# Optimization experiments

Hardware: AMD Instinct MI355X
Metric: run time of the kernel (lower is better)

Reference implementation:

```python
import jax, jax.numpy as jnp
import numpy as np

B, P, E, D, A, M, V, T = 64, 196, 2048, 512, 512, 512, 10000, 31


def setup_inputs() -> dict:
    key = jax.random.key(0)
    ks = jax.random.split(key, 20)
    s = 0.02
    inp = {
        "encoder_out": jax.random.normal(ks[0], (B, P, E), jnp.float32),
        "captions": jax.random.randint(ks[1], (B, T), 0, V),
        "caption_lengths": jax.random.randint(ks[2], (B,), 2, T + 1).at[0].set(T),
        # parameters
        "W_emb": jax.random.normal(ks[3], (V, M), jnp.float32) * s,
        "We": jax.random.normal(ks[4], (A, E), jnp.float32) * s,
        "be": jnp.zeros((A,), jnp.float32),
        "Wd": jax.random.normal(ks[5], (A, D), jnp.float32) * s,
        "bd": jnp.zeros((A,), jnp.float32),
        "wf": jax.random.normal(ks[6], (1, A), jnp.float32) * s,
        "bf": jnp.zeros((1,), jnp.float32),
        "Wih": jax.random.normal(ks[7], (4 * D, M + E), jnp.float32) * s,
        "bih": jnp.zeros((4 * D,), jnp.float32),
        "Whh": jax.random.normal(ks[8], (4 * D, D), jnp.float32) * s,
        "bhh": jnp.zeros((4 * D,), jnp.float32),
        "Wfc": jax.random.normal(ks[9], (V, D), jnp.float32) * s,
        "bfc": jnp.zeros((V,), jnp.float32),
        "Wh0": jax.random.normal(ks[10], (D, E), jnp.float32) * s,
        "bh0": jnp.zeros((D,), jnp.float32),
        "Wc0": jax.random.normal(ks[11], (D, E), jnp.float32) * s,
        "bc0": jnp.zeros((D,), jnp.float32),
    }
    return inp


def _decode(encoder_out, W_emb, We, be, Wd, bd, wf, bf, Wih, bih, Whh, bhh,
            Wfc, bfc, Wh0, bh0, Wc0, bc0, captions, caption_lengths):
    # sort by length descending (matches torch .sort(descending=True))
    idx = jnp.argsort(-caption_lengths)
    lens = caption_lengths[idx]
    enc = encoder_out[idx]              # [B,P,E]
    caps = captions[idx]                # [B,T]
    emb = W_emb[caps]                   # [B,T,M]
    mean_enc = enc.mean(axis=1)         # [B,E]
    h0 = mean_enc @ Wh0.T + bh0         # [B,D]
    c0 = mean_enc @ Wc0.T + bc0
    dec_len = lens - 1                  # [B]
    att1 = enc @ We.T + be              # [B,P,A] precomputed encoder projection
    Tmax = caps.shape[1] - 1

    def step(carry, xs):
        h, c = carry
        e_t, t = xs                     # e_t: [B,M]
        active = (t < dec_len)          # [B]
        att2 = h @ Wd.T + bd            # [B,A]
        scores = jnp.tanh(att1 + att2[:, None, :]) @ wf[0] + bf[0]  # [B,P]
        alpha = jax.nn.softmax(scores, axis=-1)                      # [B,P]
        ctx = jnp.einsum('bp,bpe->be', alpha, enc)                   # [B,E]
        x = jnp.concatenate([e_t, ctx], axis=-1)                     # [B,M+E]
        gates = x @ Wih.T + bih + h @ Whh.T + bhh                    # [B,4D]
        i_g, f_g, g_g, o_g = jnp.split(gates, 4, axis=-1)
        c_t = jax.nn.sigmoid(f_g) * c + jax.nn.sigmoid(i_g) * jnp.tanh(g_g)
        h_t = jax.nn.sigmoid(o_g) * jnp.tanh(c_t)
        pred = h_t @ Wfc.T + bfc        # dropout in eval mode = identity
        m = active[:, None]
        h_new = jnp.where(m, h_t, h)
        c_new = jnp.where(m, c_t, c)
        pred = jnp.where(m, pred, 0.0)
        alpha = jnp.where(m, alpha, 0.0)
        return (h_new, c_new), (pred, alpha)

    emb_ts = jnp.swapaxes(emb[:, :Tmax, :], 0, 1)  # [Tmax,B,M]
    ts = jnp.arange(Tmax)
    _, (preds, alphas) = jax.lax.scan(step, (h0, c0), (emb_ts, ts))
    predictions = jnp.swapaxes(preds, 0, 1)   # [B,Tmax,V]
    alphas = jnp.swapaxes(alphas, 0, 1)       # [B,Tmax,P]
    return predictions, alphas


def reference(encoder_out, captions, caption_lengths, W_emb, We, be, Wd, bd,
              wf, bf, Wih, bih, Whh, bhh, Wfc, bfc, Wh0, bh0, Wc0, bc0):
    return _decode(encoder_out, W_emb, We, be, Wd, bd, wf, bf, Wih, bih,
                   Whh, bhh, Wfc, bfc, Wh0, bh0, Wc0, bc0,
                   captions, caption_lengths)
```

## Files before the change

kernel.cpp:

```cpp
#include <hip/hip_runtime.h>
#include <cstdint>
#include <cstddef>

typedef __attribute__((ext_vector_type(8))) short short8;
typedef __attribute__((ext_vector_type(4))) float f32x4;

#define DEV static __device__ __forceinline__

#define PRED_ELEMS 19200000ULL

#define OFF_ENC   0ULL
#define OFF_ATT1  51380224ULL
#define OFF_B1    64225280ULL
#define OFF_WFC   69468160ULL
#define OFF_WEB   79724544ULL
#define OFF_B0    81821696ULL
#define OFF_HH    81821696ULL
#define OFF_B2    86016000ULL
#define OFF_HX    94404608ULL
#define OFF_C     94535680ULL
#define OFF_ATT2  94666752ULL
#define OFF_GEH   94797824ULL
#define OFF_SC    95322112ULL
#define OFF_CTX   95372288ULL
#define OFF_META  95634432ULL

DEV float b2f(unsigned short u){ unsigned v = ((unsigned)u) << 16; float f; __builtin_memcpy(&f, &v, 4); return f; }
DEV unsigned short f2b(float x){ unsigned v; __builtin_memcpy(&v, &x, 4); unsigned r = v + 0x7fffu + ((v >> 16) & 1u); return (unsigned short)(r >> 16); }
DEV float sigm(float x){ return 1.0f / (1.0f + __expf(-x)); }
DEV float tanhf_fast(float x){ float e = __expf(2.0f * x); return 1.0f - 2.0f / (e + 1.0f); }

DEV void gload16(const void* g, void* l){
  __builtin_amdgcn_global_load_lds((const __attribute__((address_space(1))) unsigned int*)g,
                                   (__attribute__((address_space(3))) unsigned int*)l, 16, 0, 0);
}

DEV void mm_core(const unsigned short* A, int ldA, int m0,
                 const unsigned short* Bm, int ldB, int n0,
                 int kIters, unsigned short* As, unsigned short* Bs, f32x4 acc[4])
{
  const int tid = threadIdx.x;
  const int lane = tid & 63, w = tid >> 6;
  const unsigned short* ga = A + (size_t)(m0 + lane) * ldA + w * 8;
  const unsigned short* gb = Bm + (size_t)(n0 + lane) * ldB + w * 8;
  unsigned short* la = As + w * 512;
  unsigned short* lb = Bs + w * 512;
  const int kb = lane >> 4, rr = lane & 15;
  for (int kk = 0; kk < kIters; ++kk) {
    gload16(ga, la); gload16(gb, lb);
    ga += 32; gb += 32;
    asm volatile("s_waitcnt vmcnt(0)" ::: "memory");
    __syncthreads();
    short8 bfr = *(const short8*)(Bs + (size_t)(kb * 64 + w * 16 + rr) * 8);
#pragma unroll
    for (int f = 0; f < 4; ++f) {
      short8 afr = *(const short8*)(As + (size_t)(kb * 64 + f * 16 + rr) * 8);
      acc[f] = __builtin_amdgcn_mfma_f32_16x16x32_bf16(afr, bfr, acc[f], 0, 0, 0);
    }
    __syncthreads();
  }
}

__global__ void k_meta(const int* __restrict__ caps, const int* __restrict__ lens, int* __restrict__ meta){
  int j = threadIdx.x;
  int lj = lens[j];
  int rank = 0;
  for (int k = 0; k < 64; ++k) { int lk = lens[k]; rank += (lk > lj) || (lk == lj && k < j); }
  meta[rank] = j; meta[64 + rank] = lj - 1;
  for (int t = 0; t < 31; ++t) meta[160 + rank * 31 + t] = caps[j * 31 + t];
  __syncthreads();
  if (j < 30) { int c = 0; for (int b = 0; b < 64; ++b) c += (meta[64 + b] > j); meta[128 + j] = c; }
}

__global__ __launch_bounds__(256) void k_encg(const float* __restrict__ enc, const int* __restrict__ meta, unsigned short* __restrict__ encb){
  int row = blockIdx.x; int b = row / 196, p = row % 196;
  const float* src = enc + ((size_t)meta[b] * 196 + p) * 2048;
  unsigned short* dst = encb + (size_t)row * 2048;
  int e0 = threadIdx.x * 8;
  short8 o;
#pragma unroll
  for (int j = 0; j < 8; ++j) o[j] = (short)f2b(src[e0 + j]);
  *(short8*)(dst + e0) = o;
}

__global__ __launch_bounds__(256) void k_wconv(const float* We, const float* Wh0, const float* Wc0,
                        const float* Wd, const float* Whh, const float* Wih, const float* Wfc,
                        unsigned short* Web, unsigned short* B0, unsigned short* B1,
                        unsigned short* Wfcb, unsigned short* B2){
  int bid = blockIdx.x, tid = threadIdx.x;
  if (bid < 512) {
    const float* s = We + (size_t)bid * 2048; unsigned short* d = Web + (size_t)bid * 2048;
    int e0 = tid * 8; short8 o;
#pragma unroll
    for (int j = 0; j < 8; ++j) o[j] = (short)f2b(s[e0 + j]);
    *(short8*)(d + e0) = o;
  } else if (bid < 1536) {
    int r = bid - 512;
    const float* s = (r < 512) ? (Wh0 + (size_t)r * 2048) : (Wc0 + (size_t)(r - 512) * 2048);
    unsigned short* d = B0 + (size_t)r * 2048;
    int e0 = tid * 8; short8 o;
#pragma unroll
    for (int j = 0; j < 8; ++j) o[j] = (short)f2b(s[e0 + j]);
    *(short8*)(d + e0) = o;
  } else if (bid < 3584) {
    int jr = bid - 1536; int g = (jr & 3) * 512 + (jr >> 2);
    const float* s = Wih + (size_t)g * 2560 + 512;
    unsigned short* d = B2 + (size_t)jr * 2048;
    int e0 = tid * 8; short8 o;
#pragma unroll
    for (int j = 0; j < 8; ++j) o[j] = (short)f2b(s[e0 + j]);
    *(short8*)(d + e0) = o;
  } else if (bid < 6144) {
    int n = bid - 3584; unsigned short* d = B1 + (size_t)n * 1024;
    int k0 = tid * 4;
    if (n < 512) {
#pragma unroll
      for (int j = 0; j < 4; ++j) { int k = k0 + j; d[k] = (k < 512) ? f2b(Wd[(size_t)n * 512 + k]) : (unsigned short)0; }
    } else {
      int j2 = n - 512; int g = (j2 & 3) * 512 + (j2 >> 2);
#pragma unroll
      for (int j = 0; j < 4; ++j) { int k = k0 + j;
        d[k] = (k < 512) ? f2b(Whh[(size_t)g * 512 + k]) : f2b(Wih[(size_t)g * 2560 + (k - 512)]); }
    }
  } else {
    int v = bid - 6144; unsigned short* d = Wfcb + (size_t)v * 512;
    int k0 = tid * 2;
#pragma unroll
    for (int j = 0; j < 2; ++j) d[k0 + j] = (v < 10000) ? f2b(Wfc[(size_t)v * 512 + k0 + j]) : (unsigned short)0;
  }
}

__global__ __launch_bounds__(256) void k_mean(const unsigned short* __restrict__ encb, unsigned short* __restrict__ meanb){
  int b = blockIdx.y, ch = blockIdx.x;
  int e = ch * 512 + threadIdx.x * 2;
  const unsigned short* ep = encb + (size_t)b * 196 * 2048 + e;
  float s0 = 0.f, s1 = 0.f;
  for (int p = 0; p < 196; ++p) {
    unsigned u = *(const unsigned*)(ep + (size_t)p * 2048);
    s0 += b2f((unsigned short)(u & 0xffff));
    s1 += b2f((unsigned short)(u >> 16));
  }
  const float inv = 1.0f / 196.0f;
  unsigned o = ((unsigned)f2b(s1 * inv) << 16) | f2b(s0 * inv);
  *(unsigned*)(meanb + (size_t)b * 2048 + e) = o;
}

__global__ __launch_bounds__(256) void k_h0c0(const unsigned short* meanb, const unsigned short* B0,
                      const float* bh0, const float* bc0, unsigned short* hx, float* cbuf){
  __shared__ __align__(16) unsigned short As[2048], Bs[2048];
  f32x4 acc[4];
#pragma unroll
  for (int f = 0; f < 4; ++f) acc[f] = (f32x4){0.f,0.f,0.f,0.f};
  int nt = blockIdx.x;
  mm_core(meanb, 2048, 0, B0, 2048, nt * 64, 64, As, Bs, acc);
  int lane = threadIdx.x & 63, w = threadIdx.x >> 6;
  int col = lane & 15, rhi = lane >> 4;
  int n = nt * 64 + w * 16 + col;
#pragma unroll
  for (int f = 0; f < 4; ++f)
#pragma unroll
    for (int r = 0; r < 4; ++r) {
      int b = f * 16 + rhi * 4 + r; float v = acc[f][r];
      if (n < 512) hx[(size_t)b * 1024 + n] = f2b(v + bh0[n]);
      else cbuf[(size_t)b * 512 + (n - 512)] = v + bc0[n - 512];
    }
}

__global__ void k_emb0(const float* __restrict__ Wemb, const int* __restrict__ meta, unsigned short* __restrict__ hx){
  int b = blockIdx.x;
  int cap = meta[160 + b * 31];
  for (int j = threadIdx.x; j < 512; j += 256)
    hx[(size_t)b * 1024 + 512 + j] = f2b(Wemb[(size_t)cap * 512 + j]);
}

__global__ __launch_bounds__(256) void k_att1(const unsigned short* __restrict__ encb,
                      const unsigned short* __restrict__ Web,
                      const float* __restrict__ be, unsigned short* __restrict__ att1b){
  __shared__ __align__(16) unsigned short As[2][4096], Bs[2][4096];
  int tid = threadIdx.x, lane = tid & 63, w = tid >> 6;
  int bid = blockIdx.x, mt, nt;
  if (bid < 384) { mt = (bid >> 5) * 8 + (bid & 7); nt = (bid >> 3) & 3; }
  else           { mt = 96 + ((bid - 384) >> 2);    nt = (bid - 384) & 3; }
  int wr = (w >> 1) * 64, wc = (w & 1) * 64;
  int rr = lane & 15, kb = lane >> 4;
  f32x4 acc[4][4];
#pragma unroll
  for (int f = 0; f < 4; ++f)
#pragma unroll
    for (int q = 0; q < 4; ++q) acc[f][q] = (f32x4){0.f,0.f,0.f,0.f};

  const unsigned short* gA = encb + (size_t)mt * 128 * 2048;
  const unsigned short* gB = Web + (size_t)nt * 128 * 2048;
  int L0 = tid, L1 = tid + 256;
  size_t s0 = (size_t)(L0 & 127) * 2048 + ((L0 >> 7) << 3);
  size_t s1 = (size_t)(L1 & 127) * 2048 + ((L1 >> 7) << 3);
  int d0 = (w * 64) * 8, d1 = (w * 64 + 256) * 8;

#define STAGE_A1(kk, bf) do { \
    gload16(gA + s0 + (size_t)(kk) * 32, &As[bf][d0]); \
    gload16(gB + s0 + (size_t)(kk) * 32, &Bs[bf][d0]); \
    gload16(gA + s1 + (size_t)(kk) * 32, &As[bf][d1]); \
    gload16(gB + s1 + (size_t)(kk) * 32, &Bs[bf][d1]); \
  } while (0)

  STAGE_A1(0, 0);
  __syncthreads();
  for (int kk = 0; kk < 64; ++kk) {
    int cur = kk & 1;
    if (kk < 63) STAGE_A1(kk + 1, cur ^ 1);
    short8 af[4], bq[4];
#pragma unroll
    for (int f = 0; f < 4; ++f)
      af[f] = *(const short8*)&As[cur][((kb << 7) + wr + f * 16 + rr) * 8];
#pragma unroll
    for (int q = 0; q < 4; ++q)
      bq[q] = *(const short8*)&Bs[cur][((kb << 7) + wc + q * 16 + rr) * 8];
#pragma unroll
    for (int f = 0; f < 4; ++f)
#pragma unroll
      for (int q = 0; q < 4; ++q)
        acc[f][q] = __builtin_amdgcn_mfma_f32_16x16x32_bf16(af[f], bq[q], acc[f][q], 0, 0, 0);
    __syncthreads();
  }
#undef STAGE_A1
  int col = lane & 15, rhi = lane >> 4;
#pragma unroll
  for (int q = 0; q < 4; ++q) {
    int n = nt * 128 + wc + q * 16 + col;
    float bev = be[n];
#pragma unroll
    for (int f = 0; f < 4; ++f)
#pragma unroll
      for (int r = 0; r < 4; ++r) {
        int m = mt * 128 + wr + f * 16 + rhi * 4 + r;
        att1b[(size_t)m * 512 + n] = f2b(acc[f][q][r] + bev);
      }
  }
}

__global__ __launch_bounds__(256) void k_step1lite(const unsigned short* __restrict__ hx,
                       const unsigned short* __restrict__ B1,
                       const float* __restrict__ bd, const float* __restrict__ bih, const float* __restrict__ bhh,
                       float* __restrict__ att2f, float* __restrict__ geh){
  int w = threadIdx.x >> 6, lane = threadIdx.x & 63;
  int omega = blockIdx.x * 4 + w;
  int rr = lane & 15, kb8 = (lane >> 4) * 8;
  const unsigned short* pb; int kIt;
  if (omega < 32) { pb = B1 + (size_t)(omega * 16 + rr) * 1024 + kb8; kIt = 16; }
  else            { pb = B1 + (size_t)(512 + (omega - 32) * 16 + rr) * 1024 + kb8; kIt = 32; }
  const unsigned short* pa0 = hx + (size_t)rr * 1024 + kb8;
  f32x4 acc[4];
#pragma unroll
  for (int f = 0; f < 4; ++f) acc[f] = (f32x4){0.f,0.f,0.f,0.f};
#pragma unroll 4
  for (int kk = 0; kk < kIt; ++kk) {
    short8 bfr = *(const short8*)(pb + kk * 32);
#pragma unroll
    for (int f = 0; f < 4; ++f) {
      short8 afr = *(const short8*)(pa0 + (size_t)f * 16384 + kk * 32);
      acc[f] = __builtin_amdgcn_mfma_f32_16x16x32_bf16(afr, bfr, acc[f], 0, 0, 0);
    }
  }
  int col = lane & 15, rhi = lane >> 4;
  if (omega < 32) {
    int n = omega * 16 + col; float bv = bd[n];
#pragma unroll
    for (int f = 0; f < 4; ++f)
#pragma unroll
      for (int r = 0; r < 4; ++r) { int b = f * 16 + rhi * 4 + r; att2f[(size_t)b * 512 + n] = acc[f][r] + bv; }
  } else {
    int j = (omega - 32) * 16 + col; int g = (j & 3) * 512 + (j >> 2);
    float bv = bih[g] + bhh[g];
#pragma unroll
    for (int f = 0; f < 4; ++f)
#pragma unroll
      for (int r = 0; r < 4; ++r) { int b = f * 16 + rhi * 4 + r; geh[(size_t)b * 2048 + j] = acc[f][r] + bv; }
  }
}

__global__ __launch_bounds__(256) void k_scores(int t, const unsigned short* __restrict__ att1b, const float* __restrict__ att2f,
                        const float* __restrict__ wf, const float* __restrict__ bfp,
                        const int* __restrict__ meta, float* __restrict__ sc){
  int b = blockIdx.y, pc = blockIdx.x;
  if (b >= meta[128 + t]) return;
  int tid = threadIdx.x, lane = tid & 63, w = tid >> 6;
  float wfr[8], a2[8];
#pragma unroll
  for (int j = 0; j < 8; ++j) { wfr[j] = wf[lane * 8 + j]; a2[j] = att2f[(size_t)b * 512 + lane * 8 + j]; }
  float bf0 = bfp[0];
  for (int pi = w; pi < 49; pi += 4) {
    int p = pc * 49 + pi;
    short8 av = *(const short8*)(att1b + ((size_t)(b * 196 + p)) * 512 + lane * 8);
    float s = 0.f;
#pragma unroll
    for (int j = 0; j < 8; ++j) s += tanhf_fast(b2f((unsigned short)av[j]) + a2[j]) * wfr[j];
#pragma unroll
    for (int off = 32; off; off >>= 1) s += __shfl_xor(s, off);
    if (lane == 0) sc[(size_t)b * 196 + p] = s + bf0;
  }
}

__global__ __launch_bounds__(256) void k_ctx(int t, const float* __restrict__ sc, const unsigned short* __restrict__ encb,
                     const int* __restrict__ meta, float* __restrict__ out, unsigned short* __restrict__ ctxb){
  int b = blockIdx.y, ch = blockIdx.x;
  if (b >= meta[128 + t]) return;
  int tid = threadIdx.x;
  __shared__ float red[256];
  __shared__ float sal[200];
  __shared__ float part[4][512];
  float v = (tid < 196) ? sc[(size_t)b * 196 + tid] : -3.0e38f;
  red[tid] = v; __syncthreads();
  for (int s = 128; s; s >>= 1) { if (tid < s) red[tid] = fmaxf(red[tid], red[tid + s]); __syncthreads(); }
  float mx = red[0]; __syncthreads();
  float ex = (tid < 196) ? __expf(v - mx) : 0.f;
  red[tid] = ex; __syncthreads();
  for (int s = 128; s; s >>= 1) { if (tid < s) red[tid] += red[tid + s]; __syncthreads(); }
  float inv = 1.0f / red[0];
  if (tid < 196) {
    float al = ex * inv;
    sal[tid] = al;
    if (ch == 0) out[PRED_ELEMS + ((size_t)b * 30 + t) * 196 + tid] = al;
  }
  __syncthreads();
  int w = tid >> 6, lane = tid & 63;
  const unsigned short* ep = encb + (size_t)b * 196 * 2048 + ch * 512 + lane * 8;
  float s8[8];
#pragma unroll
  for (int j = 0; j < 8; ++j) s8[j] = 0.f;
#pragma unroll 7
  for (int i = 0; i < 49; ++i) {
    int p = w + i * 4;
    short8 vv = *(const short8*)(ep + (size_t)p * 2048);
    float a = sal[p];
#pragma unroll
    for (int j = 0; j < 8; ++j) s8[j] += a * b2f((unsigned short)vv[j]);
  }
#pragma unroll
  for (int j = 0; j < 8; ++j) part[w][lane * 8 + j] = s8[j];
  __syncthreads();
  float r0 = part[0][tid * 2] + part[1][tid * 2] + part[2][tid * 2] + part[3][tid * 2];
  float r1 = part[0][tid * 2 + 1] + part[1][tid * 2 + 1] + part[2][tid * 2 + 1] + part[3][tid * 2 + 1];
  unsigned o = ((unsigned)f2b(r1) << 16) | f2b(r0);
  *(unsigned*)(ctxb + (size_t)b * 2048 + ch * 512 + tid * 2) = o;
}

__global__ __launch_bounds__(256) void k_step2(int t, const unsigned short* __restrict__ ctxb,
                       const unsigned short* __restrict__ B2, const float* __restrict__ geh,
                       const float* __restrict__ Wemb, const int* __restrict__ meta,
                       float* __restrict__ cbuf, unsigned short* __restrict__ hx,
                       unsigned short* __restrict__ hh){
  __shared__ float red[4][64][17];
  int w = threadIdx.x >> 6, lane = threadIdx.x & 63;
  int n0 = blockIdx.x * 16;
  int rr = lane & 15, kb8 = (lane >> 4) * 8;
  const unsigned short* pb = B2 + (size_t)(n0 + rr) * 2048 + w * 512 + kb8;
  const unsigned short* pa = ctxb + (size_t)rr * 2048 + w * 512 + kb8;
  f32x4 acc[4];
#pragma unroll
  for (int f = 0; f < 4; ++f) acc[f] = (f32x4){0.f,0.f,0.f,0.f};
#pragma unroll 4
  for (int kk = 0; kk < 16; ++kk) {
    short8 bfr = *(const short8*)(pb + kk * 32);
#pragma unroll
    for (int f = 0; f < 4; ++f) {
      short8 afr = *(const short8*)(pa + (size_t)f * 32768 + kk * 32);
      acc[f] = __builtin_amdgcn_mfma_f32_16x16x32_bf16(afr, bfr, acc[f], 0, 0, 0);
    }
  }
  int col = lane & 15, rhi = lane >> 4;
#pragma unroll
  for (int f = 0; f < 4; ++f)
#pragma unroll
    for (int r = 0; r < 4; ++r) red[w][f * 16 + rhi * 4 + r][col] = acc[f][r];
  __syncthreads();
  int b = threadIdx.x >> 2, dl = threadIdx.x & 3;
  int d = blockIdx.x * 4 + dl;
  float g4[4];
#pragma unroll
  for (int q = 0; q < 4; ++q) {
    int nl = dl * 4 + q;
    g4[q] = red[0][b][nl] + red[1][b][nl] + red[2][b][nl] + red[3][b][nl]
          + geh[(size_t)b * 2048 + n0 + nl];
  }
  float c0 = cbuf[(size_t)b * 512 + d];
  float ct = sigm(g4[1]) * c0 + sigm(g4[0]) * tanhf_fast(g4[2]);
  float ht = sigm(g4[3]) * tanhf_fast(ct);
  int na = meta[128 + t];
  unsigned short hold = hx[(size_t)b * 1024 + d];
  unsigned short hnew = (b < na) ? f2b(ht) : hold;
  if (b < na) { cbuf[(size_t)b * 512 + d] = ct; hx[(size_t)b * 1024 + d] = hnew; }
  hh[((size_t)t * 64 + b) * 512 + d] = hnew;
  int cap = meta[160 + b * 31 + t + 1];
  hx[(size_t)b * 1024 + 512 + d] = f2b(Wemb[(size_t)cap * 512 + d]);
}

__global__ __launch_bounds__(256) void k_pred(const unsigned short* __restrict__ hh,
                      const unsigned short* __restrict__ Wfcb, const float* __restrict__ bfc,
                      const int* __restrict__ meta, float* __restrict__ out){
  __shared__ __align__(16) unsigned short As[2][4096], Bs[2][4096];
  int tid = threadIdx.x, lane = tid & 63, w = tid >> 6;
  int mt = blockIdx.x % 15, nt = blockIdx.x / 15;
  int wr = (w >> 1) * 64, wc = (w & 1) * 64;
  int rr = lane & 15, kb = lane >> 4;
  f32x4 acc[4][4];
#pragma unroll
  for (int f = 0; f < 4; ++f)
#pragma unroll
    for (int q = 0; q < 4; ++q) acc[f][q] = (f32x4){0.f,0.f,0.f,0.f};

  const unsigned short* gA = hh + (size_t)mt * 128 * 512;
  int L0 = tid, L1 = tid + 256;
  size_t sa0 = (size_t)(L0 & 127) * 512 + ((L0 >> 7) << 3);
  size_t sa1 = (size_t)(L1 & 127) * 512 + ((L1 >> 7) << 3);
  int br0 = nt * 128 + (L0 & 127); if (br0 > 10015) br0 = 10015;
  int br1 = nt * 128 + (L1 & 127); if (br1 > 10015) br1 = 10015;
  size_t sb0 = (size_t)br0 * 512 + ((L0 >> 7) << 3);
  size_t sb1 = (size_t)br1 * 512 + ((L1 >> 7) << 3);
  int d0 = (w * 64) * 8, d1 = (w * 64 + 256) * 8;

#define STAGE_P(kk, bf) do { \
    gload16(gA + sa0 + (size_t)(kk) * 32, &As[bf][d0]); \
    gload16(Wfcb + sb0 + (size_t)(kk) * 32, &Bs[bf][d0]); \
    gload16(gA + sa1 + (size_t)(kk) * 32, &As[bf][d1]); \
    gload16(Wfcb + sb1 + (size_t)(kk) * 32, &Bs[bf][d1]); \
  } while (0)

  STAGE_P(0, 0);
  __syncthreads();
  for (int kk = 0; kk < 16; ++kk) {
    int cur = kk & 1;
    if (kk < 15) STAGE_P(kk + 1, cur ^ 1);
    short8 af[4], bq[4];
#pragma unroll
    for (int f = 0; f < 4; ++f)
      af[f] = *(const short8*)&As[cur][((kb << 7) + wr + f * 16 + rr) * 8];
#pragma unroll
    for (int q = 0; q < 4; ++q)
      bq[q] = *(const short8*)&Bs[cur][((kb << 7) + wc + q * 16 + rr) * 8];
#pragma unroll
    for (int f = 0; f < 4; ++f)
#pragma unroll
      for (int q = 0; q < 4; ++q)
        acc[f][q] = __builtin_amdgcn_mfma_f32_16x16x32_bf16(af[f], bq[q], acc[f][q], 0, 0, 0);
    __syncthreads();
  }
#undef STAGE_P
  int col = lane & 15, rhi = lane >> 4;
  int tt = mt * 2 + (wr >> 6);
  int na = meta[128 + tt];
#pragma unroll
  for (int q = 0; q < 4; ++q) {
    int n = nt * 128 + wc + q * 16 + col;
    if (n >= 10000) continue;
    float bv = bfc[n];
#pragma unroll
    for (int f = 0; f < 4; ++f)
#pragma unroll
      for (int r = 0; r < 4; ++r) {
        int b = f * 16 + rhi * 4 + r;
        if (b < na) out[(size_t)b * 300000 + (size_t)tt * 10000 + n] = acc[f][q][r] + bv;
      }
  }
}

extern "C" void kernel_launch(void* const* d_in, const int* in_sizes, int n_in,
                              void* d_out, int out_size, void* d_ws, size_t ws_size,
                              hipStream_t stream) {
  (void)in_sizes; (void)n_in; (void)ws_size;
  const float* enc  = (const float*)d_in[0];
  const int*   caps = (const int*)d_in[1];
  const int*   lens = (const int*)d_in[2];
  const float* Wemb = (const float*)d_in[3];
  const float* We   = (const float*)d_in[4];
  const float* be   = (const float*)d_in[5];
  const float* Wd   = (const float*)d_in[6];
  const float* bd   = (const float*)d_in[7];
  const float* wf   = (const float*)d_in[8];
  const float* bf   = (const float*)d_in[9];
  const float* Wih  = (const float*)d_in[10];
  const float* bih  = (const float*)d_in[11];
  const float* Whh  = (const float*)d_in[12];
  const float* bhh  = (const float*)d_in[13];
  const float* Wfc  = (const float*)d_in[14];
  const float* bfc  = (const float*)d_in[15];
  const float* Wh0  = (const float*)d_in[16];
  const float* bh0  = (const float*)d_in[17];
  const float* Wc0  = (const float*)d_in[18];
  const float* bc0  = (const float*)d_in[19];

  char* ws = (char*)d_ws;
  unsigned short* encb  = (unsigned short*)(ws + OFF_ENC);
  unsigned short* att1b = (unsigned short*)(ws + OFF_ATT1);
  unsigned short* B1    = (unsigned short*)(ws + OFF_B1);
  unsigned short* Wfcb  = (unsigned short*)(ws + OFF_WFC);
  unsigned short* Web   = (unsigned short*)(ws + OFF_WEB);
  unsigned short* B0    = (unsigned short*)(ws + OFF_B0);
  unsigned short* hh    = (unsigned short*)(ws + OFF_HH);
  unsigned short* B2    = (unsigned short*)(ws + OFF_B2);
  unsigned short* hx    = (unsigned short*)(ws + OFF_HX);
  float*          cbuf  = (float*)(ws + OFF_C);
  float*          att2f = (float*)(ws + OFF_ATT2);
  float*          geh   = (float*)(ws + OFF_GEH);
  float*          sc    = (float*)(ws + OFF_SC);
  unsigned short* ctxb  = (unsigned short*)(ws + OFF_CTX);
  int*            meta  = (int*)(ws + OFF_META);
  unsigned short* meanb = ctxb;
  float* out = (float*)d_out;

  hipMemsetAsync(d_out, 0, (size_t)out_size * sizeof(float), stream);
  k_meta<<<1, 64, 0, stream>>>(caps, lens, meta);
  k_encg<<<12544, 256, 0, stream>>>(enc, meta, encb);
  k_wconv<<<16160, 256, 0, stream>>>(We, Wh0, Wc0, Wd, Whh, Wih, Wfc, Web, B0, B1, Wfcb, B2);
  k_mean<<<dim3(4, 64), 256, 0, stream>>>(encb, meanb);
  k_h0c0<<<16, 256, 0, stream>>>(meanb, B0, bh0, bc0, hx, cbuf);
  k_emb0<<<64, 256, 0, stream>>>(Wemb, meta, hx);
  k_att1<<<392, 256, 0, stream>>>(encb, Web, be, att1b);
  for (int t = 0; t < 30; ++t) {
    k_step1lite<<<40, 256, 0, stream>>>(hx, B1, bd, bih, bhh, att2f, geh);
    k_scores<<<dim3(4, 64), 256, 0, stream>>>(t, att1b, att2f, wf, bf, meta, sc);
    k_ctx<<<dim3(4, 64), 256, 0, stream>>>(t, sc, encb, meta, out, ctxb);
    k_step2<<<128, 256, 0, stream>>>(t, ctxb, B2, geh, Wemb, meta, cbuf, hx, hh);
  }
  k_pred<<<1185, 256, 0, stream>>>(hh, Wfcb, bfc, meta, out);
}
```

Baseline: 1.875 ms.

## Fuse per-timestep decoder kernels into one persistent cooperative kernel with grid syncs

Replaces the 120 small per-step launches (step1, scores, ctx, step2 across 30 timesteps) with a single cooperative kernel of 256 blocks. The kernel loops over timesteps and separates phases with grid.sync. Step1 now splits its K dimension across four waves and reduces through shared memory, which spreads the work over 160 blocks instead of 40. The goal is to remove kernel launch overhead and inter-kernel gaps on the serial recurrence. In exchange it adds grid-wide barrier cost, and correctness depends on all 256 blocks being co-resident and on memory visibility through threadfence.

```diff
diff --git a/kernel.cpp b/kernel.cpp
--- a/kernel.cpp
+++ b/kernel.cpp
@@ -1,6 +1,9 @@
 #include <hip/hip_runtime.h>
+#include <hip/hip_cooperative_groups.h>
 #include <cstdint>
 #include <cstddef>
+
+namespace cg = cooperative_groups;
 
 typedef __attribute__((ext_vector_type(8))) short short8;
 typedef __attribute__((ext_vector_type(4))) float f32x4;
@@ -238,160 +241,185 @@
   }
 }
 
-__global__ __launch_bounds__(256) void k_step1lite(const unsigned short* __restrict__ hx,
-                       const unsigned short* __restrict__ B1,
-                       const float* __restrict__ bd, const float* __restrict__ bih, const float* __restrict__ bhh,
-                       float* __restrict__ att2f, float* __restrict__ geh){
-  int w = threadIdx.x >> 6, lane = threadIdx.x & 63;
-  int omega = blockIdx.x * 4 + w;
-  int rr = lane & 15, kb8 = (lane >> 4) * 8;
-  const unsigned short* pb; int kIt;
-  if (omega < 32) { pb = B1 + (size_t)(omega * 16 + rr) * 1024 + kb8; kIt = 16; }
-  else            { pb = B1 + (size_t)(512 + (omega - 32) * 16 + rr) * 1024 + kb8; kIt = 32; }
-  const unsigned short* pa0 = hx + (size_t)rr * 1024 + kb8;
-  f32x4 acc[4];
-#pragma unroll
-  for (int f = 0; f < 4; ++f) acc[f] = (f32x4){0.f,0.f,0.f,0.f};
-#pragma unroll 4
-  for (int kk = 0; kk < kIt; ++kk) {
-    short8 bfr = *(const short8*)(pb + kk * 32);
-#pragma unroll
-    for (int f = 0; f < 4; ++f) {
-      short8 afr = *(const short8*)(pa0 + (size_t)f * 16384 + kk * 32);
-      acc[f] = __builtin_amdgcn_mfma_f32_16x16x32_bf16(afr, bfr, acc[f], 0, 0, 0);
-    }
-  }
-  int col = lane & 15, rhi = lane >> 4;
-  if (omega < 32) {
-    int n = omega * 16 + col; float bv = bd[n];
-#pragma unroll
-    for (int f = 0; f < 4; ++f)
-#pragma unroll
-      for (int r = 0; r < 4; ++r) { int b = f * 16 + rhi * 4 + r; att2f[(size_t)b * 512 + n] = acc[f][r] + bv; }
-  } else {
-    int j = (omega - 32) * 16 + col; int g = (j & 3) * 512 + (j >> 2);
-    float bv = bih[g] + bhh[g];
-#pragma unroll
-    for (int f = 0; f < 4; ++f)
-#pragma unroll
-      for (int r = 0; r < 4; ++r) { int b = f * 16 + rhi * 4 + r; geh[(size_t)b * 2048 + j] = acc[f][r] + bv; }
-  }
-}
-
-__global__ __launch_bounds__(256) void k_scores(int t, const unsigned short* __restrict__ att1b, const float* __restrict__ att2f,
-                        const float* __restrict__ wf, const float* __restrict__ bfp,
-                        const int* __restrict__ meta, float* __restrict__ sc){
-  int b = blockIdx.y, pc = blockIdx.x;
-  if (b >= meta[128 + t]) return;
-  int tid = threadIdx.x, lane = tid & 63, w = tid >> 6;
-  float wfr[8], a2[8];
-#pragma unroll
-  for (int j = 0; j < 8; ++j) { wfr[j] = wf[lane * 8 + j]; a2[j] = att2f[(size_t)b * 512 + lane * 8 + j]; }
-  float bf0 = bfp[0];
-  for (int pi = w; pi < 49; pi += 4) {
-    int p = pc * 49 + pi;
-    short8 av = *(const short8*)(att1b + ((size_t)(b * 196 + p)) * 512 + lane * 8);
-    float s = 0.f;
-#pragma unroll
-    for (int j = 0; j < 8; ++j) s += tanhf_fast(b2f((unsigned short)av[j]) + a2[j]) * wfr[j];
-#pragma unroll
-    for (int off = 32; off; off >>= 1) s += __shfl_xor(s, off);
-    if (lane == 0) sc[(size_t)b * 196 + p] = s + bf0;
-  }
-}
-
-__global__ __launch_bounds__(256) void k_ctx(int t, const float* __restrict__ sc, const unsigned short* __restrict__ encb,
-                     const int* __restrict__ meta, float* __restrict__ out, unsigned short* __restrict__ ctxb){
-  int b = blockIdx.y, ch = blockIdx.x;
-  if (b >= meta[128 + t]) return;
-  int tid = threadIdx.x;
-  __shared__ float red[256];
+struct KL {
+  const unsigned short *B1, *B2, *att1b, *encb;
+  const float *bd, *bih, *bhh, *wf, *bfp, *Wemb;
+  const int* meta;
+  float *att2f, *geh, *sc;
+  unsigned short* ctxb;
+  float* cbuf;
+  unsigned short *hx, *hh;
+  float* out;
+};
+
+__global__ __launch_bounds__(256) void k_loop(KL P){
+  cg::grid_group grid = cg::this_grid();
+  const int bid = blockIdx.x, tid = threadIdx.x;
+  const int w = tid >> 6, lane = tid & 63;
+  const int rr = lane & 15, kb8 = (lane >> 4) * 8;
+  const int col = lane & 15, rhi = lane >> 4;
+  __shared__ float red[4][64][17];
   __shared__ float sal[200];
   __shared__ float part[4][512];
-  float v = (tid < 196) ? sc[(size_t)b * 196 + tid] : -3.0e38f;
-  red[tid] = v; __syncthreads();
-  for (int s = 128; s; s >>= 1) { if (tid < s) red[tid] = fmaxf(red[tid], red[tid + s]); __syncthreads(); }
-  float mx = red[0]; __syncthreads();
-  float ex = (tid < 196) ? __expf(v - mx) : 0.f;
-  red[tid] = ex; __syncthreads();
-  for (int s = 128; s; s >>= 1) { if (tid < s) red[tid] += red[tid + s]; __syncthreads(); }
-  float inv = 1.0f / red[0];
-  if (tid < 196) {
-    float al = ex * inv;
-    sal[tid] = al;
-    if (ch == 0) out[PRED_ELEMS + ((size_t)b * 30 + t) * 196 + tid] = al;
-  }
-  __syncthreads();
-  int w = tid >> 6, lane = tid & 63;
-  const unsigned short* ep = encb + (size_t)b * 196 * 2048 + ch * 512 + lane * 8;
-  float s8[8];
-#pragma unroll
-  for (int j = 0; j < 8; ++j) s8[j] = 0.f;
+  __shared__ float r256[256];
+
+  for (int t = 0; t < 30; ++t) {
+    const int na = P.meta[128 + t];
+    if (bid < 160) {
+      f32x4 acc[4];
+#pragma unroll
+      for (int f = 0; f < 4; ++f) acc[f] = (f32x4){0.f,0.f,0.f,0.f};
+      const unsigned short *pb, *pa;
+      int kIt;
+      if (bid < 32) {
+        pb = P.B1 + (size_t)(bid * 16 + rr) * 1024 + w * 128 + kb8;
+        pa = P.hx + (size_t)rr * 1024 + w * 128 + kb8;
+        kIt = 4;
+      } else {
+        int j0 = (bid - 32) * 16;
+        pb = P.B1 + (size_t)(512 + j0 + rr) * 1024 + w * 256 + kb8;
+        pa = P.hx + (size_t)rr * 1024 + w * 256 + kb8;
+        kIt = 8;
+      }
+#pragma unroll 4
+      for (int kk = 0; kk < kIt; ++kk) {
+        short8 bfr = *(const short8*)(pb + kk * 32);
+#pragma unroll
+        for (int f = 0; f < 4; ++f) {
+          short8 afr = *(const short8*)(pa + (size_t)f * 16384 + kk * 32);
+          acc[f] = __builtin_amdgcn_mfma_f32_16x16x32_bf16(afr, bfr, acc[f], 0, 0, 0);
+        }
+      }
+#pragma unroll
+      for (int f = 0; f < 4; ++f)
+#pragma unroll
+        for (int r = 0; r < 4; ++r) red[w][f * 16 + rhi * 4 + r][col] = acc[f][r];
+      __syncthreads();
+      int b = tid >> 2, dl = tid & 3;
+      if (bid < 32) {
+#pragma unroll
+        for (int q = 0; q < 4; ++q) {
+          int nl = dl * 4 + q; int n = bid * 16 + nl;
+          P.att2f[(size_t)b * 512 + n] = red[0][b][nl] + red[1][b][nl] + red[2][b][nl] + red[3][b][nl] + P.bd[n];
+        }
+      } else {
+#pragma unroll
+        for (int q = 0; q < 4; ++q) {
+          int nl = dl * 4 + q; int j = (bid - 32) * 16 + nl;
+          int g = (j & 3) * 512 + (j >> 2);
+          P.geh[(size_t)b * 2048 + j] = red[0][b][nl] + red[1][b][nl] + red[2][b][nl] + red[3][b][nl] + P.bih[g] + P.bhh[g];
+        }
+      }
+      __syncthreads();
+    }
+    __threadfence();
+    grid.sync();
+    {
+      int pc = bid & 3, b = bid >> 2;
+      if (b < na) {
+        float wfr[8], a2[8];
+#pragma unroll
+        for (int j = 0; j < 8; ++j) { wfr[j] = P.wf[lane * 8 + j]; a2[j] = P.att2f[(size_t)b * 512 + lane * 8 + j]; }
+        float bf0 = P.bfp[0];
+        for (int pi = w; pi < 49; pi += 4) {
+          int p = pc * 49 + pi;
+          short8 av = *(const short8*)(P.att1b + ((size_t)(b * 196 + p)) * 512 + lane * 8);
+          float s = 0.f;
+#pragma unroll
+          for (int j = 0; j < 8; ++j) s += tanhf_fast(b2f((unsigned short)av[j]) + a2[j]) * wfr[j];
+#pragma unroll
+          for (int off = 32; off; off >>= 1) s += __shfl_xor(s, off);
+          if (lane == 0) P.sc[(size_t)b * 196 + p] = s + bf0;
+        }
+      }
+    }
+    __threadfence();
+    grid.sync();
+    {
+      int ch = bid & 3, b = bid >> 2;
+      if (b < na) {
+        float v = (tid < 196) ? P.sc[(size_t)b * 196 + tid] : -3.0e38f;
+        r256[tid] = v; __syncthreads();
+        for (int s = 128; s; s >>= 1) { if (tid < s) r256[tid] = fmaxf(r256[tid], r256[tid + s]); __syncthreads(); }
+        float mx = r256[0]; __syncthreads();
+        float ex = (tid < 196) ? __expf(v - mx) : 0.f;
+        r256[tid] = ex; __syncthreads();
+        for (int s = 128; s; s >>= 1) { if (tid < s) r256[tid] += r256[tid + s]; __syncthreads(); }
+        float inv = 1.0f / r256[0];
+        if (tid < 196) {
+          float al = ex * inv;
+          sal[tid] = al;
+          if (ch == 0) P.out[PRED_ELEMS + ((size_t)b * 30 + t) * 196 + tid] = al;
+        }
+        __syncthreads();
+        const unsigned short* ep = P.encb + (size_t)b * 196 * 2048 + ch * 512 + lane * 8;
+        float s8[8];
+#pragma unroll
+        for (int j = 0; j < 8; ++j) s8[j] = 0.f;
 #pragma unroll 7
-  for (int i = 0; i < 49; ++i) {
-    int p = w + i * 4;
-    short8 vv = *(const short8*)(ep + (size_t)p * 2048);
-    float a = sal[p];
-#pragma unroll
-    for (int j = 0; j < 8; ++j) s8[j] += a * b2f((unsigned short)vv[j]);
-  }
-#pragma unroll
-  for (int j = 0; j < 8; ++j) part[w][lane * 8 + j] = s8[j];
-  __syncthreads();
-  float r0 = part[0][tid * 2] + part[1][tid * 2] + part[2][tid * 2] + part[3][tid * 2];
-  float r1 = part[0][tid * 2 + 1] + part[1][tid * 2 + 1] + part[2][tid * 2 + 1] + part[3][tid * 2 + 1];
-  unsigned o = ((unsigned)f2b(r1) << 16) | f2b(r0);
-  *(unsigned*)(ctxb + (size_t)b * 2048 + ch * 512 + tid * 2) = o;
-}
-
-__global__ __launch_bounds__(256) void k_step2(int t, const unsigned short* __restrict__ ctxb,
-                       const unsigned short* __restrict__ B2, const float* __restrict__ geh,
-                       const float* __restrict__ Wemb, const int* __restrict__ meta,
-                       float* __restrict__ cbuf, unsigned short* __restrict__ hx,
-                       unsigned short* __restrict__ hh){
-  __shared__ float red[4][64][17];
-  int w = threadIdx.x >> 6, lane = threadIdx.x & 63;
-  int n0 = blockIdx.x * 16;
-  int rr = lane & 15, kb8 = (lane >> 4) * 8;
-  const unsigned short* pb = B2 + (size_t)(n0 + rr) * 2048 + w * 512 + kb8;
-  const unsigned short* pa = ctxb + (size_t)rr * 2048 + w * 512 + kb8;
-  f32x4 acc[4];
-#pragma unroll
-  for (int f = 0; f < 4; ++f) acc[f] = (f32x4){0.f,0.f,0.f,0.f};
+        for (int i = 0; i < 49; ++i) {
+          int p = w + i * 4;
+          short8 vv = *(const short8*)(ep + (size_t)p * 2048);
+          float a = sal[p];
+#pragma unroll
+          for (int j = 0; j < 8; ++j) s8[j] += a * b2f((unsigned short)vv[j]);
+        }
+#pragma unroll
+        for (int j = 0; j < 8; ++j) part[w][lane * 8 + j] = s8[j];
+        __syncthreads();
+        float r0 = part[0][tid * 2] + part[1][tid * 2] + part[2][tid * 2] + part[3][tid * 2];
+        float r1 = part[0][tid * 2 + 1] + part[1][tid * 2 + 1] + part[2][tid * 2 + 1] + part[3][tid * 2 + 1];
+        unsigned o = ((unsigned)f2b(r1) << 16) | f2b(r0);
+        *(unsigned*)(P.ctxb + (size_t)b * 2048 + ch * 512 + tid * 2) = o;
+        __syncthreads();
+      }
+    }
+    __threadfence();
+    grid.sync();
+    if (bid < 128) {
+      int n0 = bid * 16;
+      const unsigned short* pb = P.B2 + (size_t)(n0 + rr) * 2048 + w * 512 + kb8;
+      const unsigned short* pa = P.ctxb + (size_t)rr * 2048 + w * 512 + kb8;
+      f32x4 acc[4];
+#pragma unroll
+      for (int f = 0; f < 4; ++f) acc[f] = (f32x4){0.f,0.f,0.f,0.f};
 #pragma unroll 4
-  for (int kk = 0; kk < 16; ++kk) {
-    short8 bfr = *(const short8*)(pb + kk * 32);
-#pragma unroll
-    for (int f = 0; f < 4; ++f) {
-      short8 afr = *(const short8*)(pa + (size_t)f * 32768 + kk * 32);
-      acc[f] = __builtin_amdgcn_mfma_f32_16x16x32_bf16(afr, bfr, acc[f], 0, 0, 0);
-    }
-  }
-  int col = lane & 15, rhi = lane >> 4;
-#pragma unroll
-  for (int f = 0; f < 4; ++f)
-#pragma unroll
-    for (int r = 0; r < 4; ++r) red[w][f * 16 + rhi * 4 + r][col] = acc[f][r];
-  __syncthreads();
-  int b = threadIdx.x >> 2, dl = threadIdx.x & 3;
-  int d = blockIdx.x * 4 + dl;
-  float g4[4];
-#pragma unroll
-  for (int q = 0; q < 4; ++q) {
-    int nl = dl * 4 + q;
-    g4[q] = red[0][b][nl] + red[1][b][nl] + red[2][b][nl] + red[3][b][nl]
-          + geh[(size_t)b * 2048 + n0 + nl];
-  }
-  float c0 = cbuf[(size_t)b * 512 + d];
-  float ct = sigm(g4[1]) * c0 + sigm(g4[0]) * tanhf_fast(g4[2]);
-  float ht = sigm(g4[3]) * tanhf_fast(ct);
-  int na = meta[128 + t];
-  unsigned short hold = hx[(size_t)b * 1024 + d];
-  unsigned short hnew = (b < na) ? f2b(ht) : hold;
-  if (b < na) { cbuf[(size_t)b * 512 + d] = ct; hx[(size_t)b * 1024 + d] = hnew; }
-  hh[((size_t)t * 64 + b) * 512 + d] = hnew;
-  int cap = meta[160 + b * 31 + t + 1];
-  hx[(size_t)b * 1024 + 512 + d] = f2b(Wemb[(size_t)cap * 512 + d]);
+      for (int kk = 0; kk < 16; ++kk) {
+        short8 bfr = *(const short8*)(pb + kk * 32);
+#pragma unroll
+        for (int f = 0; f < 4; ++f) {
+          short8 afr = *(const short8*)(pa + (size_t)f * 32768 + kk * 32);
+          acc[f] = __builtin_amdgcn_mfma_f32_16x16x32_bf16(afr, bfr, acc[f], 0, 0, 0);
+        }
+      }
+#pragma unroll
+      for (int f = 0; f < 4; ++f)
+#pragma unroll
+        for (int r = 0; r < 4; ++r) red[w][f * 16 + rhi * 4 + r][col] = acc[f][r];
+      __syncthreads();
+      int b = tid >> 2, dl = tid & 3;
+      int d = bid * 4 + dl;
+      float g4[4];
+#pragma unroll
+      for (int q = 0; q < 4; ++q) {
+        int nl = dl * 4 + q;
+        g4[q] = red[0][b][nl] + red[1][b][nl] + red[2][b][nl] + red[3][b][nl]
+              + P.geh[(size_t)b * 2048 + n0 + nl];
+      }
+      float c0 = P.cbuf[(size_t)b * 512 + d];
+      float ct = sigm(g4[1]) * c0 + sigm(g4[0]) * tanhf_fast(g4[2]);
+      float ht = sigm(g4[3]) * tanhf_fast(ct);
+      unsigned short hold = P.hx[(size_t)b * 1024 + d];
+      unsigned short hnew = (b < na) ? f2b(ht) : hold;
+      if (b < na) { P.cbuf[(size_t)b * 512 + d] = ct; P.hx[(size_t)b * 1024 + d] = hnew; }
+      P.hh[((size_t)t * 64 + b) * 512 + d] = hnew;
+      int cap = P.meta[160 + b * 31 + t + 1];
+      P.hx[(size_t)b * 1024 + 512 + d] = f2b(P.Wemb[(size_t)cap * 512 + d]);
+      __syncthreads();
+    }
+    __threadfence();
+    grid.sync();
+  }
 }
 
 __global__ __launch_bounds__(256) void k_pred(const unsigned short* __restrict__ hh,
@@ -515,11 +543,14 @@
   k_h0c0<<<16, 256, 0, stream>>>(meanb, B0, bh0, bc0, hx, cbuf);
   k_emb0<<<64, 256, 0, stream>>>(Wemb, meta, hx);
   k_att1<<<392, 256, 0, stream>>>(encb, Web, be, att1b);
-  for (int t = 0; t < 30; ++t) {
-    k_step1lite<<<40, 256, 0, stream>>>(hx, B1, bd, bih, bhh, att2f, geh);
-    k_scores<<<dim3(4, 64), 256, 0, stream>>>(t, att1b, att2f, wf, bf, meta, sc);
-    k_ctx<<<dim3(4, 64), 256, 0, stream>>>(t, sc, encb, meta, out, ctxb);
-    k_step2<<<128, 256, 0, stream>>>(t, ctxb, B2, geh, Wemb, meta, cbuf, hx, hh);
-  }
+
+  KL P;
+  P.B1 = B1; P.B2 = B2; P.att1b = att1b; P.encb = encb;
+  P.bd = bd; P.bih = bih; P.bhh = bhh; P.wf = wf; P.bfp = bf; P.Wemb = Wemb;
+  P.meta = meta; P.att2f = att2f; P.geh = geh; P.sc = sc;
+  P.ctxb = ctxb; P.cbuf = cbuf; P.hx = hx; P.hh = hh; P.out = out;
+  void* kargs[] = { &P };
+  hipLaunchCooperativeKernel((const void*)k_loop, dim3(256), dim3(256), kargs, 0, stream);
+
   k_pred<<<1185, 256, 0, stream>>>(hh, Wfcb, bfc, meta, out);
 }
```

After: 7.302 ms. +289.4%, slower.

## Precompute encoder-times-Wih projection and fuse context with LSTM gate update

Applied to the files above, without the earlier changes.

Adds a one-time GEMM that projects every encoder position through the context part of the input weights (encW = enc @ Wih_ctx^T, 12544x2048 bf16). Each step can then form the gate contributions as an alpha-weighted sum over encW rows inside one fused kernel, k_gc, which also applies the LSTM cell update. This replaces the per-step context reduction plus the separate ctx@Wih GEMM kernel, saving a launch and a GEMM on the serial path. In exchange it adds a large up-front GEMM, reads a 4x wider per-step tensor (2048 vs 512 per position), and adds bf16 rounding on the projected values. The new path is enabled only when the workspace is large enough.

```diff
diff --git a/kernel.cpp b/kernel.cpp
--- a/kernel.cpp
+++ b/kernel.cpp
@@ -24,6 +24,8 @@
 #define OFF_SC    95322112ULL
 #define OFF_CTX   95372288ULL
 #define OFF_META  95634432ULL
+#define OFF_ENCW  96000000ULL
+#define ENCW_BYTES 51380224ULL
 
 DEV float b2f(unsigned short u){ unsigned v = ((unsigned)u) << 16; float f; __builtin_memcpy(&f, &v, 4); return f; }
 DEV unsigned short f2b(float x){ unsigned v; __builtin_memcpy(&v, &x, 4); unsigned r = v + 0x7fffu + ((v >> 16) & 1u); return (unsigned short)(r >> 16); }
@@ -238,6 +240,67 @@
   }
 }
 
+__global__ __launch_bounds__(256) void k_encw(const unsigned short* __restrict__ encb,
+                      const unsigned short* __restrict__ B2, unsigned short* __restrict__ encW){
+  __shared__ __align__(16) unsigned short As[2][4096], Bs[2][4096];
+  int tid = threadIdx.x, lane = tid & 63, w = tid >> 6;
+  int mt = blockIdx.x >> 4, nt = blockIdx.x & 15;
+  int wr = (w >> 1) * 64, wc = (w & 1) * 64;
+  int rr = lane & 15, kb = lane >> 4;
+  f32x4 acc[4][4];
+#pragma unroll
+  for (int f = 0; f < 4; ++f)
+#pragma unroll
+    for (int q = 0; q < 4; ++q) acc[f][q] = (f32x4){0.f,0.f,0.f,0.f};
+
+  const unsigned short* gA = encb + (size_t)mt * 128 * 2048;
+  const unsigned short* gB = B2 + (size_t)nt * 128 * 2048;
+  int L0 = tid, L1 = tid + 256;
+  size_t s0 = (size_t)(L0 & 127) * 2048 + ((L0 >> 7) << 3);
+  size_t s1 = (size_t)(L1 & 127) * 2048 + ((L1 >> 7) << 3);
+  int d0 = (w * 64) * 8, d1 = (w * 64 + 256) * 8;
+
+#define STAGE_W(kk, bf) do { \
+    gload16(gA + s0 + (size_t)(kk) * 32, &As[bf][d0]); \
+    gload16(gB + s0 + (size_t)(kk) * 32, &Bs[bf][d0]); \
+    gload16(gA + s1 + (size_t)(kk) * 32, &As[bf][d1]); \
+    gload16(gB + s1 + (size_t)(kk) * 32, &Bs[bf][d1]); \
+  } while (0)
+
+  STAGE_W(0, 0);
+  __syncthreads();
+  for (int kk = 0; kk < 64; ++kk) {
+    int cur = kk & 1;
+    if (kk < 63) STAGE_W(kk + 1, cur ^ 1);
+    short8 af[4], bq[4];
+#pragma unroll
+    for (int f = 0; f < 4; ++f)
+      af[f] = *(const short8*)&As[cur][((kb << 7) + wr + f * 16 + rr) * 8];
+#pragma unroll
+    for (int q = 0; q < 4; ++q)
+      bq[q] = *(const short8*)&Bs[cur][((kb << 7) + wc + q * 16 + rr) * 8];
+#pragma unroll
+    for (int f = 0; f < 4; ++f)
+#pragma unroll
+      for (int q = 0; q < 4; ++q)
+        acc[f][q] = __builtin_amdgcn_mfma_f32_16x16x32_bf16(af[f], bq[q], acc[f][q], 0, 0, 0);
+    __syncthreads();
+  }
+#undef STAGE_W
+  int col = lane & 15, rhi = lane >> 4;
+#pragma unroll
+  for (int q = 0; q < 4; ++q) {
+    int n = nt * 128 + wc + q * 16 + col;
+#pragma unroll
+    for (int f = 0; f < 4; ++f)
+#pragma unroll
+      for (int r = 0; r < 4; ++r) {
+        int m = mt * 128 + wr + f * 16 + rhi * 4 + r;
+        encW[(size_t)m * 2048 + n] = f2b(acc[f][q][r]);
+      }
+  }
+}
+
 __global__ __launch_bounds__(256) void k_step1lite(const unsigned short* __restrict__ hx,
                        const unsigned short* __restrict__ B1,
                        const float* __restrict__ bd, const float* __restrict__ bih, const float* __restrict__ bhh,
@@ -297,6 +360,85 @@
 #pragma unroll
     for (int off = 32; off; off >>= 1) s += __shfl_xor(s, off);
     if (lane == 0) sc[(size_t)b * 196 + p] = s + bf0;
+  }
+}
+
+__global__ __launch_bounds__(256) void k_gc(int t, const float* __restrict__ sc,
+                      const unsigned short* __restrict__ encW, const float* __restrict__ geh,
+                      const float* __restrict__ Wemb, const int* __restrict__ meta,
+                      float* __restrict__ out, float* __restrict__ cbuf,
+                      unsigned short* __restrict__ hx, unsigned short* __restrict__ hh){
+  int b = blockIdx.y, ch = blockIdx.x;
+  int tid = threadIdx.x, lane = tid & 63, w = tid >> 6;
+  int na = meta[128 + t];
+  __shared__ float sal[200];
+  __shared__ float red[256];
+  __shared__ float part[4][512];
+  __shared__ float gt[512];
+
+  if (b < na) {
+    float v = (tid < 196) ? sc[(size_t)b * 196 + tid] : -3.0e38f;
+    red[tid] = v; __syncthreads();
+    for (int s = 128; s; s >>= 1) { if (tid < s) red[tid] = fmaxf(red[tid], red[tid + s]); __syncthreads(); }
+    float mx = red[0]; __syncthreads();
+    float ex = (tid < 196) ? __expf(v - mx) : 0.f;
+    red[tid] = ex; __syncthreads();
+    for (int s = 128; s; s >>= 1) { if (tid < s) red[tid] += red[tid + s]; __syncthreads(); }
+    float inv = 1.0f / red[0];
+    __syncthreads();
+    if (tid < 196) {
+      float al = ex * inv;
+      sal[tid] = al;
+      if (ch == 0) out[PRED_ELEMS + ((size_t)b * 30 + t) * 196 + tid] = al;
+    }
+    __syncthreads();
+
+    const unsigned short* ep = encW + ((size_t)b * 196) * 2048 + ch * 512 + lane * 8;
+    float s8[8];
+#pragma unroll
+    for (int j = 0; j < 8; ++j) s8[j] = 0.f;
+#pragma unroll 7
+    for (int i = 0; i < 49; ++i) {
+      int p = w + i * 4;
+      short8 vv = *(const short8*)(ep + (size_t)p * 2048);
+      float a = sal[p];
+#pragma unroll
+      for (int j = 0; j < 8; ++j) s8[j] += a * b2f((unsigned short)vv[j]);
+    }
+#pragma unroll
+    for (int j = 0; j < 8; ++j) part[w][lane * 8 + j] = s8[j];
+    __syncthreads();
+    int j0 = tid * 2;
+    gt[j0]     = part[0][j0] + part[1][j0] + part[2][j0] + part[3][j0]
+               + geh[(size_t)b * 2048 + ch * 512 + j0];
+    gt[j0 + 1] = part[0][j0 + 1] + part[1][j0 + 1] + part[2][j0 + 1] + part[3][j0 + 1]
+               + geh[(size_t)b * 2048 + ch * 512 + j0 + 1];
+    __syncthreads();
+
+    if (tid < 128) {
+      int d = ch * 128 + tid;
+      float ig = gt[tid * 4 + 0];
+      float fg = gt[tid * 4 + 1];
+      float gg = gt[tid * 4 + 2];
+      float og = gt[tid * 4 + 3];
+      float c0 = cbuf[(size_t)b * 512 + d];
+      float ct = sigm(fg) * c0 + sigm(ig) * tanhf_fast(gg);
+      float ht = sigm(og) * tanhf_fast(ct);
+      cbuf[(size_t)b * 512 + d] = ct;
+      unsigned short hb = f2b(ht);
+      hx[(size_t)b * 1024 + d] = hb;
+      hh[((size_t)t * 64 + b) * 512 + d] = hb;
+      int cap = meta[160 + b * 31 + t + 1];
+      hx[(size_t)b * 1024 + 512 + d] = f2b(Wemb[(size_t)cap * 512 + d]);
+    }
+  } else {
+    if (tid < 128) {
+      int d = ch * 128 + tid;
+      unsigned short hold = hx[(size_t)b * 1024 + d];
+      hh[((size_t)t * 64 + b) * 512 + d] = hold;
+      int cap = meta[160 + b * 31 + t + 1];
+      hx[(size_t)b * 1024 + 512 + d] = f2b(Wemb[(size_t)cap * 512 + d]);
+    }
   }
 }
 
@@ -466,7 +608,7 @@
 extern "C" void kernel_launch(void* const* d_in, const int* in_sizes, int n_in,
                               void* d_out, int out_size, void* d_ws, size_t ws_size,
                               hipStream_t stream) {
-  (void)in_sizes; (void)n_in; (void)ws_size;
+  (void)in_sizes; (void)n_in;
   const float* enc  = (const float*)d_in[0];
   const int*   caps = (const int*)d_in[1];
   const int*   lens = (const int*)d_in[2];
@@ -504,8 +646,11 @@
   float*          sc    = (float*)(ws + OFF_SC);
   unsigned short* ctxb  = (unsigned short*)(ws + OFF_CTX);
   int*            meta  = (int*)(ws + OFF_META);
+  unsigned short* encWb = (unsigned short*)(ws + OFF_ENCW);
   unsigned short* meanb = ctxb;
   float* out = (float*)d_out;
+
+  const bool useEncW = (ws_size >= OFF_ENCW + ENCW_BYTES);
 
   hipMemsetAsync(d_out, 0, (size_t)out_size * sizeof(float), stream);
   k_meta<<<1, 64, 0, stream>>>(caps, lens, meta);
@@ -515,11 +660,17 @@
   k_h0c0<<<16, 256, 0, stream>>>(meanb, B0, bh0, bc0, hx, cbuf);
   k_emb0<<<64, 256, 0, stream>>>(Wemb, meta, hx);
   k_att1<<<392, 256, 0, stream>>>(encb, Web, be, att1b);
+  if (useEncW) k_encw<<<1568, 256, 0, stream>>>(encb, B2, encWb);
+
   for (int t = 0; t < 30; ++t) {
     k_step1lite<<<40, 256, 0, stream>>>(hx, B1, bd, bih, bhh, att2f, geh);
     k_scores<<<dim3(4, 64), 256, 0, stream>>>(t, att1b, att2f, wf, bf, meta, sc);
-    k_ctx<<<dim3(4, 64), 256, 0, stream>>>(t, sc, encb, meta, out, ctxb);
-    k_step2<<<128, 256, 0, stream>>>(t, ctxb, B2, geh, Wemb, meta, cbuf, hx, hh);
+    if (useEncW) {
+      k_gc<<<dim3(4, 64), 256, 0, stream>>>(t, sc, encWb, geh, Wemb, meta, out, cbuf, hx, hh);
+    } else {
+      k_ctx<<<dim3(4, 64), 256, 0, stream>>>(t, sc, encb, meta, out, ctxb);
+      k_step2<<<128, 256, 0, stream>>>(t, ctxb, B2, geh, Wemb, meta, cbuf, hx, hh);
+    }
   }
   k_pred<<<1185, 256, 0, stream>>>(hh, Wfcb, bfc, meta, out);
 }
```

Result: faster. 1.804 ms (-3.8%).
